# Kernel optimization log

Measured on AMD Instinct MI355X. Metric: run time of the kernel, lower is better.

## Reference

```python
import jax, jax.numpy as jnp
import numpy as np

B, N, P, K, E = 4, 20000, 128, 128, 160000


def setup_inputs() -> dict:
    key = jax.random.key(0)
    ks = jax.random.split(key, 16)
    inv_p = 1.0 / np.sqrt(P)
    inv_3p = 1.0 / np.sqrt(3 * P)
    return {
        "x_in": jax.random.normal(ks[0], (B, N, P), jnp.float32),
        "vertex_areas": jax.random.uniform(ks[1], (B, N), jnp.float32, 1e-3, 1.0),
        "evals": jax.random.uniform(ks[2], (B, K), jnp.float32, 0.0, 10.0),
        "evecs": jax.random.normal(ks[3], (B, N, K), jnp.float32),
        "gradX_vals": jax.random.normal(ks[4], (B, E), jnp.float32),
        "gradY_vals": jax.random.normal(ks[5], (B, E), jnp.float32),
        "grad_rows": jax.random.randint(ks[6], (B, E), 0, N, jnp.int32),
        "grad_cols": jax.random.randint(ks[7], (B, E), 0, N, jnp.int32),
        # learned params
        "diffusion_times": jax.random.uniform(ks[8], (P,), jnp.float32, 1e-3, 0.1),
        "B_re": jax.random.normal(ks[9], (P, P), jnp.float32) * inv_p,
        "B_im": jax.random.normal(ks[10], (P, P), jnp.float32) * inv_p,
        "W1": jax.random.normal(ks[11], (P, 3 * P), jnp.float32) * inv_3p,
        "b1": jnp.zeros((P,), jnp.float32),
        "W2": jax.random.normal(ks[12], (P, P), jnp.float32) * inv_p,
        "b2": jnp.zeros((P,), jnp.float32),
        "W3": jax.random.normal(ks[13], (P, P), jnp.float32) * inv_p,
        "b3": jnp.zeros((P,), jnp.float32),
    }


def _spmm(rows, cols, vals, x):
    # sparse (n,n) @ dense (n,p) via COO gather/scatter
    return jax.ops.segment_sum(vals[:, None] * x[cols], rows, num_segments=x.shape[0])


def reference(x_in, vertex_areas, evals, evecs, gradX_vals, gradY_vals,
              grad_rows, grad_cols, diffusion_times, B_re, B_im,
              W1, b1, W2, b2, W3, b3):
    # SpectralDiffusion: project -> spectral heat scaling -> unproject
    times = jnp.clip(diffusion_times, 1e-8)                       # (P,)
    x_spec = jnp.einsum('bnk,bnp->bkp', evecs, x_in * vertex_areas[..., None])
    scale = jnp.exp(-evals[..., None] * times[None, None, :])     # (B,K,P)
    x_diffuse = jnp.einsum('bnk,bkp->bnp', evecs, scale * x_spec)  # (B,N,P)

    # sparse gradient halves
    gx = jax.vmap(_spmm)(grad_rows, grad_cols, gradX_vals, x_diffuse)  # (B,N,P)
    gy = jax.vmap(_spmm)(grad_rows, grad_cols, gradY_vals, x_diffuse)

    # SpatialGradient: tanh(re*B_re(re) + im*B_im(im))
    x_grad_features = jnp.tanh(gx * (gx @ B_re.T) + gy * (gy @ B_im.T))

    # MiniMLP on concatenated features (dropout inactive in eval)
    h = jnp.concatenate([x_in, x_diffuse, x_grad_features], axis=-1)  # (B,N,3P)
    h = jax.nn.relu(h @ W1.T + b1)
    h = jax.nn.relu(h @ W2.T + b2)
    h = h @ W3.T + b3
    return h + x_in
```

## Files before the change

### kernel.cpp

```cpp
#include <hip/hip_runtime.h>
#include <hip/hip_bf16.h>
#include <cstddef>

#define B_ 4
#define N_ 20000
#define P_ 128
#define K_ 128
#define E_ 160000

constexpr int NCH_S = 79;
constexpr int NSCB  = 79;

typedef __attribute__((ext_vector_type(8))) short short8;
typedef __attribute__((ext_vector_type(4))) float f32x4;

__device__ __forceinline__ unsigned pk2(float x, float y) {
  __hip_bfloat162 h = __float22bfloat162_rn(make_float2(x, y));
  union { __hip_bfloat162 h; unsigned u; } c; c.h = h; return c.u;
}
__device__ __forceinline__ float bf2f(short s) {
  union { unsigned u; float f; } c; c.u = ((unsigned)(unsigned short)s) << 16; return c.f;
}
__device__ __forceinline__ short f2bs(float x) {
  union { __hip_bfloat16 h; short s; } c; c.h = __float2bfloat16(x); return c.s;
}

__global__ __launch_bounds__(256)
void k_prep(const float* __restrict__ ev, const float* __restrict__ xin,
            const float* __restrict__ areas,
            __hip_bfloat16* __restrict__ evT, __hip_bfloat16* __restrict__ xT)
{
  const int tn = blockIdx.x, half = blockIdx.y & 1, mat = blockIdx.y >> 1;
  const int b = blockIdx.z, t = threadIdx.x;
  const int n0 = tn * 64, c0 = half * 64;
  __shared__ float ld[64][65];
  const float* src = (mat ? xin : ev) + (size_t)b * N_ * 128;
  const float* ab  = areas + (size_t)b * N_;
#pragma unroll
  for (int i = 0; i < 4; ++i) {
    int gid = t + i * 256;
    int r = gid >> 4, c4 = (gid & 15) << 2;
    int n = n0 + r;
    float4 v = make_float4(0.f, 0.f, 0.f, 0.f);
    if (n < N_) {
      v = *(const float4*)(src + (size_t)n * 128 + c0 + c4);
      if (mat == 0) { float ar = ab[n]; v.x *= ar; v.y *= ar; v.z *= ar; v.w *= ar; }
    }
    ld[r][c4] = v.x; ld[r][c4+1] = v.y; ld[r][c4+2] = v.z; ld[r][c4+3] = v.w;
  }
  __syncthreads();
  __hip_bfloat16* dst = (mat ? xT : evT) + (size_t)b * 128 * N_;
#pragma unroll
  for (int i = 0; i < 4; ++i) {
    int gid = t + i * 256;
    int cr = gid >> 4, nq = (gid & 15) << 2;
    int n = n0 + nq;
    if (n + 4 <= N_) {
      uint2 u;
      u.x = pk2(ld[nq][cr],   ld[nq+1][cr]);
      u.y = pk2(ld[nq+2][cr], ld[nq+3][cr]);
      *(uint2*)(dst + (size_t)(c0 + cr) * N_ + n) = u;
    }
  }
}

__global__ __launch_bounds__(256)
void k_wprep(const float* __restrict__ Bre, const float* __restrict__ Bim,
             uint4* __restrict__ WfRe, uint4* __restrict__ WfIm)
{
  int fid = blockIdx.x * 256 + threadIdx.x;
  if (fid >= 2048) return;
  int gg = fid >> 7, rr = fid & 127;
  const float* s0 = Bre + rr * 128 + gg * 8;
  const float* s1 = Bim + rr * 128 + gg * 8;
  float4 a0 = *(const float4*)s0, a1 = *(const float4*)(s0 + 4);
  uint4 u; u.x = pk2(a0.x, a0.y); u.y = pk2(a0.z, a0.w);
  u.z = pk2(a1.x, a1.y); u.w = pk2(a1.z, a1.w);
  WfRe[fid] = u;
  float4 b0 = *(const float4*)s1, b1 = *(const float4*)(s1 + 4);
  uint4 v; v.x = pk2(b0.x, b0.y); v.y = pk2(b0.z, b0.w);
  v.z = pk2(b1.x, b1.y); v.w = pk2(b1.z, b1.w);
  WfIm[fid] = v;
}

__global__ __launch_bounds__(256)
void k_wprep_mlp(const float* __restrict__ W1, const float* __restrict__ W2,
                 const float* __restrict__ W3, uint4* __restrict__ W1f,
                 uint4* __restrict__ W2f, uint4* __restrict__ W3f)
{
  int fid = blockIdx.x * 256 + threadIdx.x;
  if (fid >= 10240) return;
  int j = fid >> 11, wi = fid & 2047;
  int gg = wi >> 7, rr = wi & 127;
  const float* src;
  uint4* dst;
  if (j < 3)      { src = W1 + rr * 384 + j * 128 + gg * 8; dst = W1f + j * 2048 + wi; }
  else if (j == 3){ src = W2 + rr * 128 + gg * 8;           dst = W2f + wi; }
  else            { src = W3 + rr * 128 + gg * 8;           dst = W3f + wi; }
  float4 a0 = *(const float4*)src, a1 = *(const float4*)(src + 4);
  uint4 u; u.x = pk2(a0.x, a0.y); u.y = pk2(a0.z, a0.w);
  u.z = pk2(a1.x, a1.y); u.w = pk2(a1.z, a1.w);
  *dst = u;
}

__global__ __launch_bounds__(256)
void k_wprep_spec(const float* __restrict__ sspecT, uint4* __restrict__ sTf)
{
  int fid = blockIdx.x * 256 + threadIdx.x;
  if (fid >= 8192) return;
  int b = fid >> 11, wi = fid & 2047;
  int gg = wi >> 7, p = wi & 127;
  const float* src = sspecT + ((size_t)b * P_ + p) * K_ + gg * 8;
  float4 a0 = *(const float4*)src, a1 = *(const float4*)(src + 4);
  uint4 u; u.x = pk2(a0.x, a0.y); u.y = pk2(a0.z, a0.w);
  u.z = pk2(a1.x, a1.y); u.w = pk2(a1.z, a1.w);
  sTf[(size_t)b * 2048 + wi] = u;
}

__device__ __forceinline__ void stg64(uint4* __restrict__ Ls,
                                      const __hip_bfloat16* __restrict__ G,
                                      int n0, int t)
{
#pragma unroll
  for (int i = 0; i < 2; ++i) {
    int gid = t + i * 512;
    int r = gid >> 3, kg = gid & 7;
    int n = n0 + kg * 8;
    uint4 u = make_uint4(0u, 0u, 0u, 0u);
    if (n < N_) u = *(const uint4*)(G + (size_t)r * N_ + n);
    Ls[r * 8 + (kg ^ (r & 7))] = u;
  }
}

__global__ __launch_bounds__(512)
void k_spec_mm(const __hip_bfloat16* __restrict__ evT,
               const __hip_bfloat16* __restrict__ xT,
               float* __restrict__ part)
{
  const int c = blockIdx.x, b = blockIdx.y, t = threadIdx.x;
  const int l = t & 63, wid = t >> 6;
  const int wr = wid >> 2, wc = wid & 3;
  const int lr = l & 15, lg = l >> 4;
  __shared__ uint4 AsB[1024];
  __shared__ uint4 WsB[1024];
  f32x4 acc[4][2];
#pragma unroll
  for (int m = 0; m < 4; ++m)
#pragma unroll
    for (int n = 0; n < 2; ++n) acc[m][n] = (f32x4)0.f;

  const __hip_bfloat16* eb = evT + (size_t)b * 128 * N_;
  const __hip_bfloat16* xb = xT  + (size_t)b * 128 * N_;

  for (int s = 0; s < 4; ++s) {
    int n0 = c * 256 + s * 64;
    __syncthreads();
    stg64(AsB, eb, n0, t);
    stg64(WsB, xb, n0, t);
    __syncthreads();
    const short8* Ap = (const short8*)AsB;
    const short8* Wp = (const short8*)WsB;
#pragma unroll
    for (int kk = 0; kk < 2; ++kk) {
      int gg = kk * 4 + lg;
      short8 a[4], w[2];
#pragma unroll
      for (int m = 0; m < 4; ++m) { int rr = wr*64 + m*16 + lr; a[m] = Ap[rr*8 + (gg ^ (rr & 7))]; }
#pragma unroll
      for (int n = 0; n < 2; ++n) { int rr = wc*32 + n*16 + lr; w[n] = Wp[rr*8 + (gg ^ (rr & 7))]; }
#pragma unroll
      for (int m = 0; m < 4; ++m)
#pragma unroll
        for (int n = 0; n < 2; ++n)
          acc[m][n] = __builtin_amdgcn_mfma_f32_16x16x32_bf16(a[m], w[n], acc[m][n], 0, 0, 0);
    }
  }

  float* po = part + ((size_t)(b * NCH_S + c) << 14);
#pragma unroll
  for (int m = 0; m < 4; ++m)
#pragma unroll
    for (int r = 0; r < 4; ++r) {
      int row = wr*64 + m*16 + lg*4 + r;
#pragma unroll
      for (int n = 0; n < 2; ++n) {
        int col = wc*32 + n*16 + lr;
        po[row * 128 + col] = acc[m][n][r];
      }
    }
}

__global__ __launch_bounds__(256)
void k_spec_reduce(const float* __restrict__ partial, const float* __restrict__ evals,
                   const float* __restrict__ times, float* __restrict__ sspecT)
{
  int idx = blockIdx.x * 256 + threadIdx.x;
  int b = idx >> 14;
  int kp = idx & 16383;
  int k = kp >> 7, p = kp & 127;
  float s = 0.f;
  const float* pb = partial + (size_t)b * NCH_S * (K_*P_) + kp;
  for (int c = 0; c < NCH_S; ++c) s += pb[(size_t)c * (K_*P_)];
  float tt = times[p]; tt = tt < 1e-8f ? 1e-8f : tt;
  float sc = __expf(-evals[b*K_ + k] * tt);
  sspecT[((size_t)b*P_ + p) * K_ + k] = s * sc;
}

__device__ __forceinline__ void stg64r(uint4* __restrict__ Ls,
                                       const __hip_bfloat16* __restrict__ G,
                                       int nrows, int t)
{
#pragma unroll
  for (int i = 0; i < 4; ++i) {
    int gid = t + i * 256;
    int r = gid >> 4, kg = gid & 15;
    uint4 u = make_uint4(0u,0u,0u,0u);
    if (r < nrows) u = *(const uint4*)(G + (size_t)r * 128 + kg * 8);
    Ls[r * 16 + (kg ^ (r & 7))] = u;
  }
}

__device__ __forceinline__ void stg64r_f32(uint4* __restrict__ Ls,
                                           const float* __restrict__ G,
                                           int nrows, int t)
{
#pragma unroll
  for (int i = 0; i < 4; ++i) {
    int gid = t + i * 256;
    int r = gid >> 4, kg = gid & 15;
    float4 v0 = make_float4(0.f,0.f,0.f,0.f), v1 = v0;
    if (r < nrows) {
      const float* p = G + (size_t)r * 128 + kg * 8;
      v0 = *(const float4*)p;
      v1 = *(const float4*)(p + 4);
    }
    uint4 u;
    u.x = pk2(v0.x, v0.y); u.y = pk2(v0.z, v0.w);
    u.z = pk2(v1.x, v1.y); u.w = pk2(v1.z, v1.w);
    Ls[r * 16 + (kg ^ (r & 7))] = u;
  }
}

__device__ __forceinline__ void mfma_pass64(const uint4* As, const uint4* __restrict__ Wf,
                                            int wc, int lr, int lg, f32x4 acc[4][2])
{
  const short8* Ap = (const short8*)As;
  const short8* Wp = (const short8*)Wf;
#pragma unroll
  for (int kk = 0; kk < 4; ++kk) {
    int gg = kk * 4 + lg;
    short8 a[4], w[2];
#pragma unroll
    for (int m = 0; m < 4; ++m) { int rr = m*16 + lr; a[m] = Ap[rr*16 + (gg ^ (rr & 7))]; }
#pragma unroll
    for (int n = 0; n < 2; ++n) { int rr = wc*32 + n*16 + lr; w[n] = Wp[(gg << 7) + rr]; }
#pragma unroll
    for (int m = 0; m < 4; ++m)
#pragma unroll
      for (int n = 0; n < 2; ++n)
        acc[m][n] = __builtin_amdgcn_mfma_f32_16x16x32_bf16(a[m], w[n], acc[m][n], 0, 0, 0);
  }
}

__global__ __launch_bounds__(256)
void k_unproj(const float* __restrict__ evecs, const uint4* __restrict__ sTf,
              __hip_bfloat16* __restrict__ xd)
{
  const int b = blockIdx.y, r0 = blockIdx.x * 64, t = threadIdx.x;
  const int l = t & 63, w = t >> 6;
  const int lr = l & 15, lg = l >> 4;
  __shared__ uint4 LA[1024];
  f32x4 acc[4][2];
#pragma unroll
  for (int m = 0; m < 4; ++m)
#pragma unroll
    for (int n = 0; n < 2; ++n) acc[m][n] = (f32x4)0.f;
  const int nrows = min(64, N_ - r0);
  stg64r_f32(LA, evecs + (size_t)b * N_ * 128 + (size_t)r0 * 128, nrows, t);
  __syncthreads();
  mfma_pass64(LA, sTf + (size_t)b * 2048, w, lr, lg, acc);
  __hip_bfloat16* xdb = xd + (size_t)b * N_ * P_;
#pragma unroll
  for (int m = 0; m < 4; ++m)
#pragma unroll
    for (int r = 0; r < 4; ++r) {
      int row = r0 + m*16 + lg*4 + r;
      if (row >= N_) continue;
#pragma unroll
      for (int n = 0; n < 2; ++n) {
        int col = w*32 + n*16 + lr;
        xdb[(size_t)row*128 + col] = __float2bfloat16(acc[m][n][r]);
      }
    }
}

__global__ __launch_bounds__(256)
void k_grad(const uint4* __restrict__ WfRe, const uint4* __restrict__ WfIm,
            __hip_bfloat16* __restrict__ gx, const __hip_bfloat16* __restrict__ gy)
{
  const int b = blockIdx.y, r0 = blockIdx.x * 64, t = threadIdx.x;
  const int l = t & 63, wc = t >> 6;
  const int lr = l & 15, lg = l >> 4;
  __shared__ uint4 As[1024];
  __shared__ uint4 As2[1024];
  f32x4 acc1[4][2], acc2[4][2];
#pragma unroll
  for (int m = 0; m < 4; ++m)
#pragma unroll
    for (int n = 0; n < 2; ++n) { acc1[m][n] = (f32x4)0.f; acc2[m][n] = (f32x4)0.f; }

  __hip_bfloat16*       gxb = gx + (size_t)b * N_ * P_;
  const __hip_bfloat16* gyb = gy + (size_t)b * N_ * P_;
  const int nrows = min(64, N_ - r0);

  stg64r(As,  gxb + (size_t)r0 * 128, nrows, t);
  stg64r(As2, gyb + (size_t)r0 * 128, nrows, t);
  __syncthreads();
  mfma_pass64(As,  WfRe, wc, lr, lg, acc1);
  mfma_pass64(As2, WfIm, wc, lr, lg, acc2);
  __syncthreads();

  short* S1 = (short*)As;
  short* S2 = (short*)As2;
#pragma unroll
  for (int m = 0; m < 4; ++m)
#pragma unroll
    for (int r = 0; r < 4; ++r) {
      int rowt = m*16 + lg*4 + r;
#pragma unroll
      for (int n = 0; n < 2; ++n) {
        int col = wc*32 + n*16 + lr;
        int idx = (rowt*16 + ((col>>3) ^ (rowt & 7)))*8 + (col & 7);
        S1[idx] = f2bs(acc1[m][n][r]);
        S2[idx] = f2bs(acc2[m][n][r]);
      }
    }
  __syncthreads();

  {
    const int row = t >> 2, cq = t & 3;
    if (row < nrows) {
      const short8* P1 = (const short8*)As;
      const short8* P2 = (const short8*)As2;
      const size_t gbase = (size_t)(r0 + row) * 128 + cq * 32;
#pragma unroll
      for (int cg = 0; cg < 4; ++cg) {
        int kg = cq * 4 + cg;
        short8 a1 = P1[row*16 + (kg ^ (row & 7))];
        short8 a2 = P2[row*16 + (kg ^ (row & 7))];
        uint4 ux = *(const uint4*)(gxb + gbase + cg*8);
        uint4 uy = *(const uint4*)(gyb + gbase + cg*8);
        unsigned xw[4] = {ux.x, ux.y, ux.z, ux.w};
        unsigned yw[4] = {uy.x, uy.y, uy.z, uy.w};
        unsigned ow[4];
#pragma unroll
        for (int p = 0; p < 4; ++p) {
          float g1l = __uint_as_float(xw[p] << 16);
          float g1h = __uint_as_float(xw[p] & 0xffff0000u);
          float g2l = __uint_as_float(yw[p] << 16);
          float g2h = __uint_as_float(yw[p] & 0xffff0000u);
          float sl = g1l * bf2f(a1[2*p])   + g2l * bf2f(a2[2*p]);
          float sh = g1h * bf2f(a1[2*p+1]) + g2h * bf2f(a2[2*p+1]);
          sl = fminf(fmaxf(sl, -15.f), 15.f);
          sh = fminf(fmaxf(sh, -15.f), 15.f);
          float el = __expf(2.f * sl), eh = __expf(2.f * sh);
          ow[p] = pk2((el - 1.f) / (el + 1.f), (eh - 1.f) / (eh + 1.f));
        }
        uint4 o; o.x = ow[0]; o.y = ow[1]; o.z = ow[2]; o.w = ow[3];
        *(uint4*)(gxb + gbase + cg*8) = o;
      }
    }
  }
}

__global__ __launch_bounds__(256)
void k_mlp(const float* __restrict__ xin, const __hip_bfloat16* __restrict__ xd,
           const __hip_bfloat16* __restrict__ xg,
           const uint4* __restrict__ W1f, const uint4* __restrict__ W2f,
           const uint4* __restrict__ W3f,
           const float* __restrict__ b1, const float* __restrict__ b2,
           const float* __restrict__ b3, float* __restrict__ out)
{
  const int b = blockIdx.y, r0 = blockIdx.x * 64, t = threadIdx.x;
  const int l = t & 63, w = t >> 6;
  const int lr = l & 15, lg = l >> 4;
  __shared__ uint4 LA0[1024];
  __shared__ uint4 LA1[1024];
  __shared__ uint4 LA2[1024];
  __shared__ uint4 LB[1024];
  const int nrows = min(64, N_ - r0);
  const float* xinb = xin + (size_t)b * N_ * 128 + (size_t)r0 * 128;

  stg64r_f32(LA0, xinb, nrows, t);
  stg64r(LA1, xd + (size_t)b * N_ * 128 + (size_t)r0 * 128, nrows, t);
  stg64r(LA2, xg + (size_t)b * N_ * 128 + (size_t)r0 * 128, nrows, t);
  __syncthreads();

  f32x4 acc[4][2];
#pragma unroll
  for (int m = 0; m < 4; ++m)
#pragma unroll
    for (int n = 0; n < 2; ++n) acc[m][n] = (f32x4)0.f;
  mfma_pass64(LA0, W1f,        w, lr, lg, acc);
  mfma_pass64(LA1, W1f + 2048, w, lr, lg, acc);
  mfma_pass64(LA2, W1f + 4096, w, lr, lg, acc);

  {
    float bb[2] = { b1[w*32 + lr], b1[w*32 + 16 + lr] };
    short* Sh = (short*)LB;
#pragma unroll
    for (int m = 0; m < 4; ++m)
#pragma unroll
      for (int r = 0; r < 4; ++r) {
        int rowt = m*16 + lg*4 + r;
#pragma unroll
        for (int n = 0; n < 2; ++n) {
          int col = w*32 + n*16 + lr;
          float v = fmaxf(acc[m][n][r] + bb[n], 0.f);
          Sh[(rowt*16 + ((col>>3) ^ (rowt & 7)))*8 + (col & 7)] = f2bs(v);
        }
      }
  }
  __syncthreads();

#pragma unroll
  for (int m = 0; m < 4; ++m)
#pragma unroll
    for (int n = 0; n < 2; ++n) acc[m][n] = (f32x4)0.f;
  mfma_pass64(LB, W2f, w, lr, lg, acc);
  __syncthreads();
  {
    float bb[2] = { b2[w*32 + lr], b2[w*32 + 16 + lr] };
    short* Sh = (short*)LB;
#pragma unroll
    for (int m = 0; m < 4; ++m)
#pragma unroll
      for (int r = 0; r < 4; ++r) {
        int rowt = m*16 + lg*4 + r;
#pragma unroll
        for (int n = 0; n < 2; ++n) {
          int col = w*32 + n*16 + lr;
          float v = fmaxf(acc[m][n][r] + bb[n], 0.f);
          Sh[(rowt*16 + ((col>>3) ^ (rowt & 7)))*8 + (col & 7)] = f2bs(v);
        }
      }
  }
  __syncthreads();

#pragma unroll
  for (int m = 0; m < 4; ++m)
#pragma unroll
    for (int n = 0; n < 2; ++n) acc[m][n] = (f32x4)0.f;
  mfma_pass64(LB, W3f, w, lr, lg, acc);
  {
    float bb[2] = { b3[w*32 + lr], b3[w*32 + 16 + lr] };
    float* ob = out + (size_t)b * N_ * 128;
#pragma unroll
    for (int m = 0; m < 4; ++m)
#pragma unroll
      for (int r = 0; r < 4; ++r) {
        int row = r0 + m*16 + lg*4 + r;
        if (row >= N_) continue;
#pragma unroll
        for (int n = 0; n < 2; ++n) {
          int col = w*32 + n*16 + lr;
          float v = acc[m][n][r] + bb[n] + xinb[(size_t)(m*16 + lg*4 + r)*128 + col];
          ob[(size_t)row*128 + col] = v;
        }
      }
  }
}

__global__ void k_count(const int* __restrict__ rows, int* __restrict__ cnt)
{
  int b = blockIdx.y;
  int e = blockIdx.x * 256 + threadIdx.x;
  if (e < E_) atomicAdd(&cnt[b*N_ + rows[(size_t)b*E_ + e]], 1);
}

__global__ __launch_bounds__(256)
void k_scan_blk(const int* __restrict__ cnt, int* __restrict__ off,
                int* __restrict__ bsum)
{
  const int c = blockIdx.x, b = blockIdx.y, t = threadIdx.x;
  const int lane = t & 63, wid = t >> 6;
  __shared__ int wt[4];
  int i = c * 256 + t;
  int v = (i < N_) ? cnt[b*N_ + i] : 0;
  int x = v;
#pragma unroll
  for (int ofs = 1; ofs < 64; ofs <<= 1) {
    int y = __shfl_up(x, ofs, 64);
    if (lane >= ofs) x += y;
  }
  if (lane == 63) wt[wid] = x;
  __syncthreads();
  int wofs = 0;
  for (int wj = 0; wj < wid; ++wj) wofs += wt[wj];
  if (i < N_) off[b*(N_+1) + i] = wofs + x - v;
  if (t == 255) bsum[b*128 + c] = wofs + x;
}

__global__ __launch_bounds__(64)
void k_scan_top(int* __restrict__ bsum, int* __restrict__ off)
{
  const int b = blockIdx.x, t = threadIdx.x;
  int running = 0;
  for (int base = 0; base < 128; base += 64) {
    int i = base + t;
    int v = (i < NSCB) ? bsum[b*128 + i] : 0;
    int x = v;
#pragma unroll
    for (int ofs = 1; ofs < 64; ofs <<= 1) {
      int y = __shfl_up(x, ofs, 64);
      if (t >= ofs) x += y;
    }
    if (i < 128) bsum[b*128 + i] = running + x - v;
    running += __shfl(x, 63, 64);
  }
  if (t == 0) off[b*(N_+1) + N_] = running;
}

__global__ __launch_bounds__(256)
void k_scan_add(const int* __restrict__ bsum, int* __restrict__ off,
                int* __restrict__ pos)
{
  const int c = blockIdx.x, b = blockIdx.y;
  int i = c * 256 + (int)threadIdx.x;
  if (i < N_) {
    int o = off[b*(N_+1) + i] + bsum[b*128 + c];
    off[b*(N_+1) + i] = o;
    pos[b*N_ + i] = o;
  }
}

__global__ void k_fill(const int* __restrict__ rows, const int* __restrict__ cols,
                       const float* __restrict__ vx, const float* __restrict__ vy,
                       int* __restrict__ pos, uint4* __restrict__ prec)
{
  int b = blockIdx.y;
  int e = blockIdx.x * 256 + threadIdx.x;
  if (e < E_) {
    size_t be = (size_t)b*E_ + e;
    int r = rows[be];
    int p = atomicAdd(&pos[b*N_ + r], 1);
    if (p >= 0 && p < E_) {
      uint4 rec;
      rec.x = (unsigned)cols[be];
      rec.y = __float_as_uint(vx[be]);
      rec.z = __float_as_uint(vy[be]);
      rec.w = 0u;
      prec[(size_t)b*E_ + p] = rec;
    }
  }
}

__global__ __launch_bounds__(256)
void k_gather(const __hip_bfloat16* __restrict__ xd, const uint4* __restrict__ prec,
              const int* __restrict__ off,
              __hip_bfloat16* __restrict__ gx, __hip_bfloat16* __restrict__ gy)
{
  const int b = blockIdx.y;
  const int row = (blockIdx.x * 256 + threadIdx.x) >> 6;
  const int lane = threadIdx.x & 63;
  const int q = lane >> 4, ql = lane & 15;
  if (row >= N_) return;
  const int s = off[b*(N_+1) + row], e = off[b*(N_+1) + row + 1];
  float ax[8], ay[8];
#pragma unroll
  for (int k = 0; k < 8; ++k) { ax[k] = 0.f; ay[k] = 0.f; }
  const __hip_bfloat16* xdb = xd + (size_t)b * N_ * P_;
  const uint4* pb = prec + (size_t)b * E_;

  for (int i = s; i < e; i += 8) {
    int idx0 = i + q, idx1 = i + 4 + q;
    bool v0 = idx0 < e, v1 = idx1 < e;
    uint4 rec0 = pb[v0 ? idx0 : (e - 1)];
    uint4 rec1 = pb[v1 ? idx1 : (e - 1)];
    float fx0 = v0 ? __uint_as_float(rec0.y) : 0.f;
    float fy0 = v0 ? __uint_as_float(rec0.z) : 0.f;
    float fx1 = v1 ? __uint_as_float(rec1.y) : 0.f;
    float fy1 = v1 ? __uint_as_float(rec1.z) : 0.f;
    uint4 va = *(const uint4*)(xdb + (size_t)rec0.x * P_ + ql * 8);
    uint4 vb = *(const uint4*)(xdb + (size_t)rec1.x * P_ + ql * 8);
    unsigned aw[4] = {va.x, va.y, va.z, va.w};
    unsigned bw[4] = {vb.x, vb.y, vb.z, vb.w};
#pragma unroll
    for (int p = 0; p < 4; ++p) {
      float a_lo = __uint_as_float(aw[p] << 16);
      float a_hi = __uint_as_float(aw[p] & 0xffff0000u);
      float b_lo = __uint_as_float(bw[p] << 16);
      float b_hi = __uint_as_float(bw[p] & 0xffff0000u);
      ax[2*p]   = fmaf(fx0, a_lo, ax[2*p]);   ax[2*p]   = fmaf(fx1, b_lo, ax[2*p]);
      ax[2*p+1] = fmaf(fx0, a_hi, ax[2*p+1]); ax[2*p+1] = fmaf(fx1, b_hi, ax[2*p+1]);
      ay[2*p]   = fmaf(fy0, a_lo, ay[2*p]);   ay[2*p]   = fmaf(fy1, b_lo, ay[2*p]);
      ay[2*p+1] = fmaf(fy0, a_hi, ay[2*p+1]); ay[2*p+1] = fmaf(fy1, b_hi, ay[2*p+1]);
    }
  }
#pragma unroll
  for (int k = 0; k < 8; ++k) {
    ax[k] += __shfl_xor(ax[k], 16, 64); ax[k] += __shfl_xor(ax[k], 32, 64);
    ay[k] += __shfl_xor(ay[k], 16, 64); ay[k] += __shfl_xor(ay[k], 32, 64);
  }
  if (lane < 16) {
    size_t o = (size_t)b * N_ * P_ + (size_t)row * P_ + ql * 8;
    uint4 ux, uy;
    ux.x = pk2(ax[0], ax[1]); ux.y = pk2(ax[2], ax[3]);
    ux.z = pk2(ax[4], ax[5]); ux.w = pk2(ax[6], ax[7]);
    uy.x = pk2(ay[0], ay[1]); uy.y = pk2(ay[2], ay[3]);
    uy.z = pk2(ay[4], ay[5]); uy.w = pk2(ay[6], ay[7]);
    *(uint4*)(gx + o) = ux;
    *(uint4*)(gy + o) = uy;
  }
}

extern "C" void kernel_launch(void* const* d_in, const int* in_sizes, int n_in,
                              void* d_out, int out_size, void* d_ws, size_t ws_size,
                              hipStream_t stream)
{
  const float* x_in  = (const float*)d_in[0];
  const float* areas = (const float*)d_in[1];
  const float* evals = (const float*)d_in[2];
  const float* evecs = (const float*)d_in[3];
  const float* gXv   = (const float*)d_in[4];
  const float* gYv   = (const float*)d_in[5];
  const int*   grows = (const int*)d_in[6];
  const int*   gcols = (const int*)d_in[7];
  const float* times = (const float*)d_in[8];
  const float* Bre   = (const float*)d_in[9];
  const float* Bim   = (const float*)d_in[10];
  const float* W1    = (const float*)d_in[11];
  const float* b1    = (const float*)d_in[12];
  const float* W2    = (const float*)d_in[13];
  const float* b2    = (const float*)d_in[14];
  const float* W3    = (const float*)d_in[15];
  const float* b3    = (const float*)d_in[16];

  float* ws = (float*)d_ws;
  __hip_bfloat16* xd_bf = (__hip_bfloat16*)ws;
  float*          part  = ws + 6000000;
  __hip_bfloat16* gx_bf = (__hip_bfloat16*)(ws + 12000000);
  __hip_bfloat16* gy_bf = (__hip_bfloat16*)(ws + 18000000);
  __hip_bfloat16* evT   = gx_bf;
  __hip_bfloat16* xT    = gy_bf;

  uint4* prec   = (uint4*)(ws + 24000000);
  int*   ipos   = (int*)(ws + 26560000);
  int*   ioff   = ipos + B_*N_;
  float* sspecT = ws + 26750000;
  uint4* WfRe   = (uint4*)(ws + 26816000);
  uint4* WfIm   = WfRe + 2048;
  int*   bsum   = (int*)(WfIm + 2048);
  uint4* W1f    = (uint4*)(ws + 26834000);
  uint4* W2f    = W1f + 6144;
  uint4* W3f    = W2f + 2048;
  uint4* sTf    = W3f + 2048;
  float* out    = (float*)d_out;

  const int TN = (N_ + 63) / 64;

  k_prep<<<dim3(TN, 4, B_), 256, 0, stream>>>(evecs, x_in, areas, evT, xT);
  k_wprep<<<dim3(8), 256, 0, stream>>>(Bre, Bim, WfRe, WfIm);
  k_wprep_mlp<<<dim3(40), 256, 0, stream>>>(W1, W2, W3, W1f, W2f, W3f);
  k_spec_mm<<<dim3(NCH_S, B_), 512, 0, stream>>>(evT, xT, part);
  k_spec_reduce<<<dim3(B_*K_*P_/256), 256, 0, stream>>>(part, evals, times, sspecT);
  k_wprep_spec<<<dim3(32), 256, 0, stream>>>(sspecT, sTf);
  k_unproj<<<dim3(TN, B_), 256, 0, stream>>>(evecs, sTf, xd_bf);
  hipMemsetAsync(ipos, 0, (size_t)B_*N_*sizeof(int), stream);
  k_count<<<dim3(E_/256, B_), 256, 0, stream>>>(grows, ipos);
  k_scan_blk<<<dim3(NSCB, B_), 256, 0, stream>>>(ipos, ioff, bsum);
  k_scan_top<<<dim3(B_), 64, 0, stream>>>(bsum, ioff);
  k_scan_add<<<dim3(NSCB, B_), 256, 0, stream>>>(bsum, ioff, ipos);
  k_fill<<<dim3(E_/256, B_), 256, 0, stream>>>(grows, gcols, gXv, gYv, ipos, prec);
  k_gather<<<dim3(N_/4, B_), 256, 0, stream>>>(xd_bf, prec, ioff, gx_bf, gy_bf);
  k_grad<<<dim3(TN, B_), 256, 0, stream>>>(WfRe, WfIm, gx_bf, gy_bf);
  k_mlp<<<dim3(TN, B_), 256, 0, stream>>>(x_in, xd_bf, gx_bf, W1f, W2f, W3f,
                                          b1, b2, b3, out);
}
```

Measured before the change: 246.9 us.

## Restructure MLP kernel so each wave owns 16 rows with direct-from-global A loads

```diff
diff --git a/kernel.cpp b/kernel.cpp
--- a/kernel.cpp
+++ b/kernel.cpp
@@ -384,90 +384,112 @@
   const int b = blockIdx.y, r0 = blockIdx.x * 64, t = threadIdx.x;
   const int l = t & 63, w = t >> 6;
   const int lr = l & 15, lg = l >> 4;
-  __shared__ uint4 LA0[1024];
-  __shared__ uint4 LA1[1024];
-  __shared__ uint4 LA2[1024];
-  __shared__ uint4 LB[1024];
-  const int nrows = min(64, N_ - r0);
-  const float* xinb = xin + (size_t)b * N_ * 128 + (size_t)r0 * 128;
-
-  stg64r_f32(LA0, xinb, nrows, t);
-  stg64r(LA1, xd + (size_t)b * N_ * 128 + (size_t)r0 * 128, nrows, t);
-  stg64r(LA2, xg + (size_t)b * N_ * 128 + (size_t)r0 * 128, nrows, t);
-  __syncthreads();
-
-  f32x4 acc[4][2];
-#pragma unroll
-  for (int m = 0; m < 4; ++m)
-#pragma unroll
-    for (int n = 0; n < 2; ++n) acc[m][n] = (f32x4)0.f;
-  mfma_pass64(LA0, W1f,        w, lr, lg, acc);
-  mfma_pass64(LA1, W1f + 2048, w, lr, lg, acc);
-  mfma_pass64(LA2, W1f + 4096, w, lr, lg, acc);
-
+  __shared__ uint4 H[4][256];
+  uint4* Hw = H[w];
+  const short8* Hp = (const short8*)Hw;
+  short* Hs = (short*)Hw;
+
+  const int rbase = r0 + w * 16;
+  const int arow  = min(rbase + lr, N_ - 1);
+  const size_t boff = (size_t)b * N_ * 128;
+  const float* xinb = xin + boff;
+
+  f32x4 acc[8];
+#pragma unroll
+  for (int n = 0; n < 8; ++n) acc[n] = (f32x4)0.f;
+
+#pragma unroll
+  for (int kk = 0; kk < 4; ++kk) {
+    const float* p = xinb + (size_t)arow * 128 + kk * 32 + lg * 8;
+    float4 v0 = *(const float4*)p, v1 = *(const float4*)(p + 4);
+    union { uint4 u; short8 s; } af;
+    af.u.x = pk2(v0.x, v0.y); af.u.y = pk2(v0.z, v0.w);
+    af.u.z = pk2(v1.x, v1.y); af.u.w = pk2(v1.z, v1.w);
+    const int kg = (kk << 2) + lg;
+#pragma unroll
+    for (int n = 0; n < 8; ++n) {
+      union { uint4 u; short8 s; } wf; wf.u = W1f[(kg << 7) + n*16 + lr];
+      acc[n] = __builtin_amdgcn_mfma_f32_16x16x32_bf16(af.s, wf.s, acc[n], 0, 0, 0);
+    }
+  }
+#pragma unroll
+  for (int c = 1; c < 3; ++c) {
+    const __hip_bfloat16* src = (c == 1 ? xd : xg) + boff;
+#pragma unroll
+    for (int kk = 0; kk < 4; ++kk) {
+      union { uint4 u; short8 s; } af;
+      af.u = *(const uint4*)(src + (size_t)arow * 128 + kk * 32 + lg * 8);
+      const int kg = (kk << 2) + lg;
+#pragma unroll
+      for (int n = 0; n < 8; ++n) {
+        union { uint4 u; short8 s; } wf; wf.u = W1f[(c << 11) + (kg << 7) + n*16 + lr];
+        acc[n] = __builtin_amdgcn_mfma_f32_16x16x32_bf16(af.s, wf.s, acc[n], 0, 0, 0);
+      }
+    }
+  }
+
+#pragma unroll
+  for (int n = 0; n < 8; ++n) {
+    float bb = b1[n*16 + lr];
+#pragma unroll
+    for (int r = 0; r < 4; ++r) {
+      int rowt = lg*4 + r;
+      int col = n*16 + lr;
+      float v = fmaxf(acc[n][r] + bb, 0.f);
+      Hs[(rowt*16 + ((col>>3) ^ (rowt & 7)))*8 + (col & 7)] = f2bs(v);
+    }
+  }
+
+#pragma unroll
+  for (int n = 0; n < 8; ++n) acc[n] = (f32x4)0.f;
+#pragma unroll
+  for (int kk = 0; kk < 4; ++kk) {
+    const int kg = (kk << 2) + lg;
+    short8 a = Hp[lr*16 + (kg ^ (lr & 7))];
+#pragma unroll
+    for (int n = 0; n < 8; ++n) {
+      union { uint4 u; short8 s; } wf; wf.u = W2f[(kg << 7) + n*16 + lr];
+      acc[n] = __builtin_amdgcn_mfma_f32_16x16x32_bf16(a, wf.s, acc[n], 0, 0, 0);
+    }
+  }
+#pragma unroll
+  for (int n = 0; n < 8; ++n) {
+    float bb = b2[n*16 + lr];
+#pragma unroll
+    for (int r = 0; r < 4; ++r) {
+      int rowt = lg*4 + r;
+      int col = n*16 + lr;
+      float v = fmaxf(acc[n][r] + bb, 0.f);
+      Hs[(rowt*16 + ((col>>3) ^ (rowt & 7)))*8 + (col & 7)] = f2bs(v);
+    }
+  }
+
+#pragma unroll
+  for (int n = 0; n < 8; ++n) acc[n] = (f32x4)0.f;
+#pragma unroll
+  for (int kk = 0; kk < 4; ++kk) {
+    const int kg = (kk << 2) + lg;
+    short8 a = Hp[lr*16 + (kg ^ (lr & 7))];
+#pragma unroll
+    for (int n = 0; n < 8; ++n) {
+      union { uint4 u; short8 s; } wf; wf.u = W3f[(kg << 7) + n*16 + lr];
+      acc[n] = __builtin_amdgcn_mfma_f32_16x16x32_bf16(a, wf.s, acc[n], 0, 0, 0);
+    }
+  }
   {
-    float bb[2] = { b1[w*32 + lr], b1[w*32 + 16 + lr] };
-    short* Sh = (short*)LB;
-#pragma unroll
-    for (int m = 0; m < 4; ++m)
+    float* ob = out + boff;
+#pragma unroll
+    for (int n = 0; n < 8; ++n) {
+      float bb = b3[n*16 + lr];
 #pragma unroll
       for (int r = 0; r < 4; ++r) {
-        int rowt = m*16 + lg*4 + r;
-#pragma unroll
-        for (int n = 0; n < 2; ++n) {
-          int col = w*32 + n*16 + lr;
-          float v = fmaxf(acc[m][n][r] + bb[n], 0.f);
-          Sh[(rowt*16 + ((col>>3) ^ (rowt & 7)))*8 + (col & 7)] = f2bs(v);
-        }
+        int row = rbase + lg*4 + r;
+        if (row >= N_) continue;
+        int col = n*16 + lr;
+        float v = acc[n][r] + bb + xinb[(size_t)row*128 + col];
+        ob[(size_t)row*128 + col] = v;
       }
-  }
-  __syncthreads();
-
-#pragma unroll
-  for (int m = 0; m < 4; ++m)
-#pragma unroll
-    for (int n = 0; n < 2; ++n) acc[m][n] = (f32x4)0.f;
-  mfma_pass64(LB, W2f, w, lr, lg, acc);
-  __syncthreads();
-  {
-    float bb[2] = { b2[w*32 + lr], b2[w*32 + 16 + lr] };
-    short* Sh = (short*)LB;
-#pragma unroll
-    for (int m = 0; m < 4; ++m)
-#pragma unroll
-      for (int r = 0; r < 4; ++r) {
-        int rowt = m*16 + lg*4 + r;
-#pragma unroll
-        for (int n = 0; n < 2; ++n) {
-          int col = w*32 + n*16 + lr;
-          float v = fmaxf(acc[m][n][r] + bb[n], 0.f);
-          Sh[(rowt*16 + ((col>>3) ^ (rowt & 7)))*8 + (col & 7)] = f2bs(v);
-        }
-      }
-  }
-  __syncthreads();
-
-#pragma unroll
-  for (int m = 0; m < 4; ++m)
-#pragma unroll
-    for (int n = 0; n < 2; ++n) acc[m][n] = (f32x4)0.f;
-  mfma_pass64(LB, W3f, w, lr, lg, acc);
-  {
-    float bb[2] = { b3[w*32 + lr], b3[w*32 + 16 + lr] };
-    float* ob = out + (size_t)b * N_ * 128;
-#pragma unroll
-    for (int m = 0; m < 4; ++m)
-#pragma unroll
-      for (int r = 0; r < 4; ++r) {
-        int row = r0 + m*16 + lg*4 + r;
-        if (row >= N_) continue;
-#pragma unroll
-        for (int n = 0; n < 2; ++n) {
-          int col = w*32 + n*16 + lr;
-          float v = acc[m][n][r] + bb[n] + xinb[(size_t)(m*16 + lg*4 + r)*128 + col];
-          ob[(size_t)row*128 + col] = v;
-        }
-      }
+    }
   }
 }
 
```

Measured after the change: 246.0 us. Within noise of the previous version (-0.4%).
